# Kernel optimization log

Hardware: AMD Instinct MI355X
Metric: run time of the kernel (lower is better)

The kernel has to match this reference:

```python
import jax, jax.numpy as jnp
import numpy as np

TEMPERATURE = 0.5
TAU_PLUS = 0.1
EPS = 1e-8


def setup_inputs() -> dict:
    key = jax.random.key(0)
    k1, k2 = jax.random.split(key)
    B, D = 8192, 128
    z_i = jax.random.normal(k1, (B, D), dtype=jnp.float32)
    z_j = jax.random.normal(k2, (B, D), dtype=jnp.float32)
    return {"z_i": z_i, "z_j": z_j}


def _l2_normalize(x, axis=1, eps=1e-12):
    # matches torch F.normalize: x / max(||x||, eps)
    n = jnp.linalg.norm(x, axis=axis, keepdims=True)
    return x / jnp.maximum(n, eps)


def reference(z_i, z_j):
    B = z_i.shape[0]
    zi = _l2_normalize(z_i, axis=1)
    zj = _l2_normalize(z_j, axis=1)
    reps = jnp.concatenate([zi, zj], axis=0)  # [2B, D]
    sim = jnp.matmul(reps, reps.T) / TEMPERATURE  # [2B, 2B]
    sim = sim - jnp.max(sim, axis=1, keepdims=True)
    mask = jnp.eye(2 * B, dtype=bool)
    sim = jnp.where(mask, -9e15, sim)
    pos = jnp.exp(jnp.sum(zi * zj, axis=-1) / TEMPERATURE)  # [B]
    positives = jnp.concatenate([pos, pos], axis=0)  # [2B]
    neg_sum = jnp.sum(jnp.exp(sim), axis=1)  # [2B]
    Ng = (-TAU_PLUS * B * positives + neg_sum) / (1.0 - TAU_PLUS)
    Ng = jnp.maximum(Ng, B * jnp.exp(jnp.asarray(-1.0 / TEMPERATURE, dtype=sim.dtype)))
    loss = -jnp.log(positives / (positives + Ng + EPS))
    return jnp.mean(loss)
```

## Files before the change

kernel.cpp:

```cpp
#include <hip/hip_runtime.h>
#include <hip/hip_bf16.h>

typedef __attribute__((ext_vector_type(8))) short bf16x8;
typedef __attribute__((ext_vector_type(4))) float f32x4;

#define B_ROWS 8192
#define NROWS 16384
#define D 128
#define C1 2.8853900817779268f
#define E_M2 0.13533528323661270f
#define RSCALE 1.6986436f
#define TILE_COLS 64
#define TILE_BYTES (TILE_COLS * D * 2)
#define SMAX 32
#define NBLK 1056
#define NSLICE 8

__device__ __forceinline__ float fast_exp2(float x) {
#if __has_builtin(__builtin_amdgcn_exp2f)
    return __builtin_amdgcn_exp2f(x);
#else
    float r; asm("v_exp_f32 %0, %1" : "=v"(r) : "v"(x)); return r;
#endif
}
__device__ __forceinline__ float fast_log2(float x) {
#if __has_builtin(__builtin_amdgcn_logf)
    return __builtin_amdgcn_logf(x);
#else
    float r; asm("v_log_f32 %0, %1" : "=v"(r) : "v"(x)); return r;
#endif
}

__device__ __forceinline__ unsigned short f2bf(float f) {
    union { float f; unsigned u; } v; v.f = f;
    unsigned r = v.u + 0x7FFFu + ((v.u >> 16) & 1u);
    return (unsigned short)(r >> 16);
}

__device__ __host__ __forceinline__ int colpart_off(int I) {
    return I * NROWS - 128 * I * (I + 1);
}

__global__ __launch_bounds__(256) void k_norm(const float* __restrict__ zi,
                                              const float* __restrict__ zj,
                                              unsigned* __restrict__ repsU,
                                              float* __restrict__ pos) {
    int w = threadIdx.x >> 6, lane = threadIdx.x & 63;
    int row = blockIdx.x * 4 + w;
    const float2* a2 = (const float2*)(zi + (size_t)row * D);
    const float2* b2 = (const float2*)(zj + (size_t)row * D);
    float2 a = a2[lane], b = b2[lane];
    float si = a.x * a.x + a.y * a.y;
    float sj = b.x * b.x + b.y * b.y;
    float sd = a.x * b.x + a.y * b.y;
#pragma unroll
    for (int m = 32; m; m >>= 1) {
        si += __shfl_xor(si, m);
        sj += __shfl_xor(sj, m);
        sd += __shfl_xor(sd, m);
    }
    float inv_i = 1.0f / fmaxf(sqrtf(si), 1e-12f);
    float inv_j = 1.0f / fmaxf(sqrtf(sj), 1e-12f);
    float sa = inv_i * RSCALE, sb = inv_j * RSCALE;
    repsU[(size_t)row * 64 + lane] =
        (unsigned)f2bf(a.x * sa) | ((unsigned)f2bf(a.y * sa) << 16);
    repsU[(size_t)(row + B_ROWS) * 64 + lane] =
        (unsigned)f2bf(b.x * sb) | ((unsigned)f2bf(b.y * sb) << 16);
    if (lane == 0) pos[row] = fast_exp2(sd * inv_i * inv_j * C1);
}

__global__ __launch_bounds__(256, 2) void k_negsum(const unsigned short* __restrict__ R,
                                                   float* __restrict__ rowpart,
                                                   float* __restrict__ colpart) {
    __shared__ char smem[2][TILE_BYTES];
    __shared__ float colredL[2][4][64];
    int b = blockIdx.x, I = 0;
    for (;;) { int S = 32 - (I >> 1); if (b < S) break; b -= S; ++I; }
    int s = b;
    int S_I = 32 - (I >> 1);
    int rowBase = I << 8;
    int jstart = (I << 2) + s;
    int L_I = 256 - (I << 2);
    int nt = (L_I - s + S_I - 1) / S_I;

    int w = threadIdx.x >> 6;
    int lane = threadIdx.x & 63;
    int lr = lane & 15, lk = lane >> 4;
    int waveRow = rowBase + w * 64;

    bf16x8 afrag[4][4];
#pragma unroll
    for (int r = 0; r < 4; ++r)
#pragma unroll
        for (int kk = 0; kk < 4; ++kk)
            afrag[r][kk] = *(const bf16x8*)(R + (size_t)(waveRow + r * 16 + lr) * D + kk * 32 + lk * 8);

    int srcoff[4], dstoff[4];
#pragma unroll
    for (int j = 0; j < 4; ++j) {
        int o = (w * 4 + j) * 1024 + lane * 16;
        int row = o >> 8, c = o & 255;
        srcoff[j] = row * 256 + (c ^ ((row & 7) << 4));
        dstoff[j] = (w * 4 + j) * 1024;
    }

    const char* Rb = (const char*)R;

    int m64 = (lr & 4) << 4;
    int lbase = lr * 256 + ((lk * 16) ^ ((lr & 3) << 4));

    float acc[4][4] = {};

#define STAGE(buf, jj)                                                            \
    do {                                                                          \
        const char* tb_ = Rb + (size_t)(jj) * (TILE_COLS * 256);                  \
        _Pragma("unroll")                                                         \
        for (int j = 0; j < 4; ++j)                                               \
            __builtin_amdgcn_global_load_lds(                                     \
                (const __attribute__((address_space(1))) unsigned*)(tb_ + srcoff[j]), \
                (__attribute__((address_space(3))) unsigned*)(&smem[buf][dstoff[j]]), \
                16, 0, 0);                                                        \
    } while (0)

#define BATCH_BODY(DIAG)                                                          \
    do {                                                                          \
        _Pragma("unroll")                                                         \
        for (int ct = 0; ct < 4; ++ct) {                                          \
            _Pragma("unroll")                                                     \
            for (int r = 0; r < 4; ++r) {                                         \
                f32x4 c = {0.f, 0.f, 0.f, 0.f};                                   \
                c = __builtin_amdgcn_mfma_f32_16x16x32_bf16(afrag[r][0], bf[ct][0], c, 0, 0, 0); \
                c = __builtin_amdgcn_mfma_f32_16x16x32_bf16(afrag[r][1], bf[ct][1], c, 0, 0, 0); \
                c = __builtin_amdgcn_mfma_f32_16x16x32_bf16(afrag[r][2], bf[ct][2], c, 0, 0, 0); \
                c = __builtin_amdgcn_mfma_f32_16x16x32_bf16(afrag[r][3], bf[ct][3], c, 0, 0, 0); \
                if (DIAG && ct == r) {                                            \
                    _Pragma("unroll")                                             \
                    for (int q = 0; q < 4; ++q)                                   \
                        if (lk * 4 + q != lr) {                                   \
                            float e = fast_exp2(c[q]);                            \
                            acc[r][q] += e; csum[ct] += e;                        \
                        }                                                         \
                } else {                                                          \
                    _Pragma("unroll")                                             \
                    for (int q = 0; q < 4; ++q) {                                 \
                        float e = fast_exp2(c[q]);                                \
                        acc[r][q] += e; csum[ct] += e;                            \
                    }                                                             \
                }                                                                 \
            }                                                                     \
        }                                                                         \
    } while (0)

    STAGE(0, jstart);
    __syncthreads();
    int cur = 0;
    int prevColBase = -1, prevBuf = 0;
    for (int t = 0; t < nt; ++t) {
        int jt = jstart + t * S_I;
        int colBase = jt << 6;
        if (prevColBase >= 0 && w == ((t + 3) & 3)) {
            float v = colredL[prevBuf][0][lane] + colredL[prevBuf][1][lane] +
                      colredL[prevBuf][2][lane] + colredL[prevBuf][3][lane];
            colpart[colpart_off(I) + prevColBase + lane - ((I + 1) << 8)] = v;
        }
        if (t + 1 < nt) STAGE(cur ^ 1, jt + S_I);
        const char* sb = &smem[cur][0] + lbase;
        bf16x8 bf[4][4];
#pragma unroll
        for (int ct = 0; ct < 4; ++ct)
#pragma unroll
            for (int kk = 0; kk < 4; ++kk)
                bf[ct][kk] = *(const bf16x8*)(sb + ct * 4096 + ((kk * 64) ^ m64));
        float csum[4] = {0.f, 0.f, 0.f, 0.f};
        bool offdiag = (colBase >= rowBase + 256);
        if (colBase == waveRow) {
            BATCH_BODY(true);
        } else {
            BATCH_BODY(false);
        }
        if (offdiag) {
#pragma unroll
            for (int ct = 0; ct < 4; ++ct) {
                float v = csum[ct];
                v += __shfl_xor(v, 16);
                v += __shfl_xor(v, 32);
                if (lk == 0) colredL[cur][w][ct * 16 + lr] = v;
            }
        }
        __syncthreads();
        prevColBase = offdiag ? colBase : -1;
        prevBuf = cur;
        cur ^= 1;
    }
    if (prevColBase >= 0 && w == ((nt + 3) & 3)) {
        float v = colredL[prevBuf][0][lane] + colredL[prevBuf][1][lane] +
                  colredL[prevBuf][2][lane] + colredL[prevBuf][3][lane];
        colpart[colpart_off(I) + prevColBase + lane - ((I + 1) << 8)] = v;
    }
#undef STAGE
#undef BATCH_BODY

#pragma unroll
    for (int r = 0; r < 4; ++r)
#pragma unroll
        for (int q = 0; q < 4; ++q) {
            float v = acc[r][q];
            v += __shfl_xor(v, 1);
            v += __shfl_xor(v, 2);
            v += __shfl_xor(v, 4);
            v += __shfl_xor(v, 8);
            if (lr == 0)
                rowpart[(size_t)s * NROWS + waveRow + r * 16 + lk * 4 + q] = v;
        }
}

__global__ __launch_bounds__(256) void k_negred(const float* __restrict__ rowpart,
                                                const float* __restrict__ colpart,
                                                float* __restrict__ negp) {
    int g = blockIdx.x >> 3;
    int z = blockIdx.x & (NSLICE - 1);
    int i = g * 256 + threadIdx.x;
    int S_I = 32 - (g >> 1);
    float a = 0.f;
    for (int s = z; s < S_I; s += NSLICE)
        a += rowpart[(size_t)s * NROWS + i];
    for (int I = z; I < g; I += NSLICE)
        a += colpart[colpart_off(I) + i - ((I + 1) << 8)];
    negp[(size_t)z * NROWS + i] = a;
}

__global__ __launch_bounds__(256) void k_loss1(const float* __restrict__ pos,
                                               const float* __restrict__ negp,
                                               float* __restrict__ bsum) {
    int i = blockIdx.x * 256 + threadIdx.x;
    float neg = 0.f;
#pragma unroll
    for (int z = 0; z < NSLICE; ++z) neg += negp[(size_t)z * NROWS + i];
    neg *= E_M2;
    float p = pos[i & (B_ROWS - 1)];
    float Ng = fmaxf((neg - 819.2f * p) * (1.0f / 0.9f), 8192.0f * E_M2);
    float l = fast_log2((p + Ng + 1e-8f) / p) * 0.69314718056f;
#pragma unroll
    for (int m = 32; m; m >>= 1) l += __shfl_xor(l, m);
    __shared__ float s4[4];
    int wv = threadIdx.x >> 6;
    if ((threadIdx.x & 63) == 0) s4[wv] = l;
    __syncthreads();
    if (threadIdx.x == 0) bsum[blockIdx.x] = s4[0] + s4[1] + s4[2] + s4[3];
}

__global__ void k_loss2(const float* __restrict__ bsum, float* __restrict__ out) {
    float v = bsum[threadIdx.x];
#pragma unroll
    for (int m = 32; m; m >>= 1) v += __shfl_xor(v, m);
    if (threadIdx.x == 0) out[0] = v * (1.0f / (float)NROWS);
}

extern "C" void kernel_launch(void* const* d_in, const int* in_sizes, int n_in,
                              void* d_out, int out_size, void* d_ws, size_t ws_size,
                              hipStream_t stream) {
    const float* zi = (const float*)d_in[0];
    const float* zj = (const float*)d_in[1];
    char* ws = (char*)d_ws;
    unsigned short* reps = (unsigned short*)ws;
    float* pos = (float*)(ws + 4194304);
    float* rowpart = pos + B_ROWS;
    float* colpart = rowpart + (size_t)SMAX * NROWS;
    float* negp = colpart + 516096;
    float* bsum = negp + (size_t)NSLICE * NROWS;
    float* out = (float*)d_out;

    k_norm<<<B_ROWS / 4, 256, 0, stream>>>(zi, zj, (unsigned*)reps, pos);
    k_negsum<<<NBLK, 256, 0, stream>>>(reps, rowpart, colpart);
    k_negred<<<64 * NSLICE, 256, 0, stream>>>(rowpart, colpart, negp);
    k_loss1<<<NROWS / 256, 256, 0, stream>>>(pos, negp, bsum);
    k_loss2<<<1, 64, 0, stream>>>(bsum, out);
}
```

Baseline: 78.93 us.

## Use fixed 16-way column split with phase-aligned tiles and LDS column reduction

Replaces the variable per-row-band split (32 down to 17 slices, 1056 blocks) with a fixed 16-way split (1024 blocks), where each block's starting column tile is phase-shifted so tiles are assigned mod 16. The goal is a simpler block-to-work mapping and fewer rowpart partials, at the cost of less even per-block work, since some blocks get zero or few tiles. Column-sum reduction drops the cross-lane shuffles: each lane writes its raw partial into a larger LDS array, and the consuming wave later sums 16 values, trading shuffles for extra LDS traffic. Blocks whose work is empty now skip staging.

```diff
diff --git a/kernel.cpp b/kernel.cpp
--- a/kernel.cpp
+++ b/kernel.cpp
@@ -12,8 +12,8 @@
 #define RSCALE 1.6986436f
 #define TILE_COLS 64
 #define TILE_BYTES (TILE_COLS * D * 2)
-#define SMAX 32
-#define NBLK 1056
+#define NSPLIT 16
+#define NBLK (64 * NSPLIT)
 #define NSLICE 8
 
 __device__ __forceinline__ float fast_exp2(float x) {
@@ -73,15 +73,13 @@
                                                    float* __restrict__ rowpart,
                                                    float* __restrict__ colpart) {
     __shared__ char smem[2][TILE_BYTES];
-    __shared__ float colredL[2][4][64];
-    int b = blockIdx.x, I = 0;
-    for (;;) { int S = 32 - (I >> 1); if (b < S) break; b -= S; ++I; }
-    int s = b;
-    int S_I = 32 - (I >> 1);
+    __shared__ float colacc[2][4][4][80];
+    int I = blockIdx.x >> 4;
+    int s = blockIdx.x & (NSPLIT - 1);
     int rowBase = I << 8;
-    int jstart = (I << 2) + s;
-    int L_I = 256 - (I << 2);
-    int nt = (L_I - s + S_I - 1) / S_I;
+    int dph = (s - ((I << 2) & 15)) & 15;
+    int jstart = (I << 2) + dph;
+    int nt = (jstart < 256) ? (((255 - jstart) >> 4) + 1) : 0;
 
     int w = threadIdx.x >> 6;
     int lane = threadIdx.x & 63;
@@ -151,19 +149,23 @@
         }                                                                         \
     } while (0)
 
-    STAGE(0, jstart);
+    if (nt > 0) STAGE(0, jstart);
     __syncthreads();
     int cur = 0;
-    int prevColBase = -1, prevBuf = 0;
     for (int t = 0; t < nt; ++t) {
-        int jt = jstart + t * S_I;
+        int jt = jstart + (t << 4);
         int colBase = jt << 6;
-        if (prevColBase >= 0 && w == ((t + 3) & 3)) {
-            float v = colredL[prevBuf][0][lane] + colredL[prevBuf][1][lane] +
-                      colredL[prevBuf][2][lane] + colredL[prevBuf][3][lane];
-            colpart[colpart_off(I) + prevColBase + lane - ((I + 1) << 8)] = v;
-        }
-        if (t + 1 < nt) STAGE(cur ^ 1, jt + S_I);
+        if (t > 0 && w == ((t + 3) & 3)) {
+            int pcb = colBase - 1024;
+            if (pcb >= rowBase + 256) {
+                int par = (t - 1) & 1;
+                float v = 0.f;
+#pragma unroll
+                for (int u = 0; u < 16; ++u) v += colacc[par][u >> 2][u & 3][lane];
+                colpart[colpart_off(I) + pcb + lane - ((I + 1) << 8)] = v;
+            }
+        }
+        if (t + 1 < nt) STAGE(cur ^ 1, jt + 16);
         const char* sb = &smem[cur][0] + lbase;
         bf16x8 bf[4][4];
 #pragma unroll
@@ -179,23 +181,23 @@
             BATCH_BODY(false);
         }
         if (offdiag) {
-#pragma unroll
-            for (int ct = 0; ct < 4; ++ct) {
-                float v = csum[ct];
-                v += __shfl_xor(v, 16);
-                v += __shfl_xor(v, 32);
-                if (lk == 0) colredL[cur][w][ct * 16 + lr] = v;
-            }
+            int par = t & 1;
+#pragma unroll
+            for (int ct = 0; ct < 4; ++ct)
+                colacc[par][w][lk][ct * 16 + lr] = csum[ct];
         }
         __syncthreads();
-        prevColBase = offdiag ? colBase : -1;
-        prevBuf = cur;
         cur ^= 1;
     }
-    if (prevColBase >= 0 && w == ((nt + 3) & 3)) {
-        float v = colredL[prevBuf][0][lane] + colredL[prevBuf][1][lane] +
-                  colredL[prevBuf][2][lane] + colredL[prevBuf][3][lane];
-        colpart[colpart_off(I) + prevColBase + lane - ((I + 1) << 8)] = v;
+    if (nt > 0 && w == ((nt + 3) & 3)) {
+        int pcb = (jstart + ((nt - 1) << 4)) << 6;
+        if (pcb >= rowBase + 256) {
+            int par = (nt - 1) & 1;
+            float v = 0.f;
+#pragma unroll
+            for (int u = 0; u < 16; ++u) v += colacc[par][u >> 2][u & 3][lane];
+            colpart[colpart_off(I) + pcb + lane - ((I + 1) << 8)] = v;
+        }
     }
 #undef STAGE
 #undef BATCH_BODY
@@ -220,9 +222,9 @@
     int g = blockIdx.x >> 3;
     int z = blockIdx.x & (NSLICE - 1);
     int i = g * 256 + threadIdx.x;
-    int S_I = 32 - (g >> 1);
     float a = 0.f;
-    for (int s = z; s < S_I; s += NSLICE)
+#pragma unroll
+    for (int s = z; s < NSPLIT; s += NSLICE)
         a += rowpart[(size_t)s * NROWS + i];
     for (int I = z; I < g; I += NSLICE)
         a += colpart[colpart_off(I) + i - ((I + 1) << 8)];
@@ -265,7 +267,7 @@
     unsigned short* reps = (unsigned short*)ws;
     float* pos = (float*)(ws + 4194304);
     float* rowpart = pos + B_ROWS;
-    float* colpart = rowpart + (size_t)SMAX * NROWS;
+    float* colpart = rowpart + (size_t)NSPLIT * NROWS;
     float* negp = colpart + 516096;
     float* bsum = negp + (size_t)NSLICE * NROWS;
     float* out = (float*)d_out;
```

Result: faster. 65.93 us (-16.5%).
